# Kernel tuning notes

Hardware: AMD Instinct MI355X
Metric: run time of the kernel (lower is better)

The kernel has to match this reference:

```python
import jax, jax.numpy as jnp
import numpy as np

SLOT = 32
MLP_H = 128
N_SLOTS = 7
N_ITER = 3
EPS = 1e-8
SCALE = SLOT ** -0.5
LN_EPS = 1e-5  # torch LayerNorm default


def _ln(x, g, b):
    m = jnp.mean(x, axis=-1, keepdims=True)
    v = jnp.var(x, axis=-1, keepdims=True)
    return (x - m) * jax.lax.rsqrt(v + LN_EPS) * g + b


def setup_inputs() -> dict:
    key = jax.random.key(0)
    ks = jax.random.split(key, 16)
    def w(k, shape, fan_in):
        return jax.random.normal(k, shape, jnp.float32) * (1.0 / np.sqrt(fan_in))
    return {
        "inputs": jax.random.normal(ks[0], (64, 4096, MLP_H), jnp.float32),
        "slots_init": jax.random.normal(ks[1], (64, N_SLOTS, SLOT), jnp.float32),
        "ln_in_g": jnp.ones((MLP_H,), jnp.float32),
        "ln_in_b": jnp.zeros((MLP_H,), jnp.float32),
        "Wk": w(ks[2], (SLOT, MLP_H), MLP_H),
        "Wv": w(ks[3], (SLOT, MLP_H), MLP_H),
        "Wq": w(ks[4], (SLOT, SLOT), SLOT),
        "ln_s_g": jnp.ones((SLOT,), jnp.float32),
        "ln_s_b": jnp.zeros((SLOT,), jnp.float32),
        "gru_wi": w(ks[5], (3 * SLOT, SLOT), SLOT),
        "gru_wh": w(ks[6], (3 * SLOT, SLOT), SLOT),
        "gru_bi": jnp.zeros((3 * SLOT,), jnp.float32),
        "gru_bh": jnp.zeros((3 * SLOT,), jnp.float32),
        "ln_m_g": jnp.ones((SLOT,), jnp.float32),
        "ln_m_b": jnp.zeros((SLOT,), jnp.float32),
        "mlp_w1": w(ks[7], (MLP_H, SLOT), SLOT),
        "mlp_b1": jnp.zeros((MLP_H,), jnp.float32),
        "mlp_w2": w(ks[8], (SLOT, MLP_H), MLP_H),
        "mlp_b2": jnp.zeros((SLOT,), jnp.float32),
    }


def _gru_cell(x, h, wi, wh, bi, bh):
    # torch.nn.GRUCell math; gate order r, z, n
    gi = x @ wi.T + bi
    gh = h @ wh.T + bh
    gi_r, gi_z, gi_n = jnp.split(gi, 3, axis=-1)
    gh_r, gh_z, gh_n = jnp.split(gh, 3, axis=-1)
    r = jax.nn.sigmoid(gi_r + gh_r)
    z = jax.nn.sigmoid(gi_z + gh_z)
    n = jnp.tanh(gi_n + r * gh_n)
    return (1.0 - z) * n + z * h


def reference(inputs, slots_init, ln_in_g, ln_in_b, Wk, Wv, Wq, ln_s_g, ln_s_b,
              gru_wi, gru_wh, gru_bi, gru_bh, ln_m_g, ln_m_b,
              mlp_w1, mlp_b1, mlp_w2, mlp_b2):
    x = _ln(inputs, ln_in_g, ln_in_b)           # [B, N, 128]
    k = x @ Wk.T                                # [B, N, 32]
    v = x @ Wv.T                                # [B, N, 32]

    slots = slots_init                          # [B, S, 32]
    attn = None
    for m in range(N_ITER + 1):
        slots_prev = slots
        s = _ln(slots, ln_s_g, ln_s_b)
        q = s @ Wq.T                            # [B, S, 32]
        dots = jnp.einsum('bid,bjd->bij', q, k) * SCALE   # [B, S, N]
        attn = jax.nn.softmax(dots, axis=1) + EPS          # softmax over slots
        attn = attn / jnp.sum(attn, axis=-1, keepdims=True)
        updates = jnp.einsum('bjd,bij->bid', v, attn)      # [B, S, 32]
        slots = _gru_cell(updates, slots_prev, gru_wi, gru_wh, gru_bi, gru_bh)
        h = _ln(slots, ln_m_g, ln_m_b)
        h = jax.nn.relu(h @ mlp_w1.T + mlp_b1) @ mlp_w2.T + mlp_b2
        slots = slots + h
        if m == N_ITER - 1:
            slots = jax.lax.stop_gradient(slots)
    return slots, attn, slots
```

## Files before the change

kernel.cpp:

```cpp
#include <hip/hip_runtime.h>
#include <stdint.h>

#define B_   64
#define N_   4096
#define H_   128
#define S_   7
#define D_   32
#define SCALE_ 0.17677669529663687f
#define EPS_   1e-8f
#define LNEPS_ 1e-5f
#define AUS_ 260

typedef __bf16 bf16x8 __attribute__((ext_vector_type(8)));
typedef float  floatx4 __attribute__((ext_vector_type(4)));

__device__ __forceinline__ uint32_t cvt2(float a, float b){
  union { __bf16 h[2]; uint32_t u; } r;
  r.h[0] = (__bf16)a; r.h[1] = (__bf16)b;
  return r.u;
}
__device__ __forceinline__ float bfLO(uint32_t u){ union{uint32_t i; float f;} x; x.i = u << 16;         return x.f; }
__device__ __forceinline__ float bfHI(uint32_t u){ union{uint32_t i; float f;} x; x.i = u & 0xffff0000u; return x.f; }
__device__ __forceinline__ void up8(uint4 u, float* o){
  o[0]=bfLO(u.x); o[1]=bfHI(u.x); o[2]=bfLO(u.y); o[3]=bfHI(u.y);
  o[4]=bfLO(u.z); o[5]=bfHI(u.z); o[6]=bfLO(u.w); o[7]=bfHI(u.w);
}

__global__ __launch_bounds__(256) void init_w(const float* __restrict__ Wk, const float* __restrict__ Wv,
                                              const float* __restrict__ g,  const float* __restrict__ bta,
                                              uint16_t* __restrict__ fragbuf,
                                              float* __restrict__ c1arr, float* __restrict__ c2arr){
  int tid = blockIdx.x * 256 + threadIdx.x;
  if (blockIdx.x < 4){
    int nt = tid >> 8, kc = (tid >> 6) & 3, l = tid & 63;
    int col = (nt & 1) * 16 + (l & 15);
    int dbase = kc * 32 + (l >> 4) * 8;
    const float* wr = (nt < 2 ? Wk : Wv) + col * 128 + dbase;
    const float* gr = g + dbase;
    uint32_t u[4];
    #pragma unroll
    for (int j = 0; j < 4; ++j)
      u[j] = cvt2(wr[2*j] * gr[2*j], wr[2*j+1] * gr[2*j+1]);
    *reinterpret_cast<uint4*>(fragbuf + (size_t)tid * 8) = make_uint4(u[0], u[1], u[2], u[3]);
  } else {
    int t = threadIdx.x;
    if (t < 128){
      int which = t >> 5, col = t & 31;
      const float* Wb  = (which & 2) ? Wv : Wk;
      const float* vec = (which & 1) ? bta : g;
      float a = 0.f;
      for (int d = 0; d < 128; ++d) a += vec[d] * Wb[col * 128 + d];
      float* dst = (which & 1) ? c2arr : c1arr;
      dst[(which >> 1) * 32 + col] = a;
    }
  }
}

__global__ __launch_bounds__(256) void ln_kv(const float* __restrict__ x,
                                             const uint16_t* __restrict__ fragbuf,
                                             const float* __restrict__ c1arr, const float* __restrict__ c2arr,
                                             uint16_t* __restrict__ kb, uint16_t* __restrict__ vb){
  __shared__ union {
    uint16_t atile[64 * 136];
    float    rep[4352];
  } sh;
  __shared__ float2 stats[32 * 65];
  __shared__ float2 rowstat[64];
  int t = threadIdx.x;
  int l = t & 63, w = t >> 6;
  size_t rowbase = (size_t)blockIdx.x * 64;

  bf16x8 bfr[4][4];
  #pragma unroll
  for (int nt = 0; nt < 4; ++nt)
    #pragma unroll
    for (int kc = 0; kc < 4; ++kc)
      bfr[nt][kc] = *reinterpret_cast<const bf16x8*>(fragbuf + (((nt * 4 + kc) * 64 + l) * 8));

  float c1c[4], c2c[4];
  #pragma unroll
  for (int nt = 0; nt < 4; ++nt){
    int colk = (nt & 1) * 16 + (l & 15);
    c1c[nt] = c1arr[(nt >> 1) * 32 + colk];
    c2c[nt] = c2arr[(nt >> 1) * 32 + colk];
  }

  const float4* xp = reinterpret_cast<const float4*>(x + rowbase * H_);
  #pragma unroll
  for (int k = 0; k < 8; ++k){
    float4 v = xp[k * 256 + t];
    int row = 8 * k + (t >> 5);
    uint32_t lo = cvt2(v.x, v.y);
    uint32_t hi = cvt2(v.z, v.w);
    *reinterpret_cast<uint2*>(&sh.atile[row * 136 + (t & 31) * 4]) = make_uint2(lo, hi);
    float s  = v.x + v.y + v.z + v.w;
    float s2 = v.x*v.x + v.y*v.y + v.z*v.z + v.w*v.w;
    stats[(t & 31) * 65 + row] = make_float2(s, s2);
  }
  __syncthreads();

  {
    int row = t >> 2, q = t & 3;
    float s = 0.f, s2 = 0.f;
    #pragma unroll
    for (int j = 0; j < 8; ++j){
      float2 p = stats[(q * 8 + j) * 65 + row];
      s += p.x; s2 += p.y;
    }
    s  += __shfl_xor(s, 1);  s2 += __shfl_xor(s2, 1);
    s  += __shfl_xor(s, 2);  s2 += __shfl_xor(s2, 2);
    if (q == 0){
      float mean = s * (1.f / 128.f);
      float var  = s2 * (1.f / 128.f) - mean * mean;
      float rstd = rsqrtf(var + LNEPS_);
      rowstat[row] = make_float2(rstd, -mean * rstd);
    }
  }
  __syncthreads();

  floatx4 acc[4] = {{0,0,0,0},{0,0,0,0},{0,0,0,0},{0,0,0,0}};
  #pragma unroll
  for (int kc = 0; kc < 4; ++kc){
    bf16x8 afr = *reinterpret_cast<const bf16x8*>(
        &sh.atile[(w * 16 + (l & 15)) * 136 + kc * 32 + (l >> 4) * 8]);
    #pragma unroll
    for (int nt = 0; nt < 4; ++nt)
      acc[nt] = __builtin_amdgcn_mfma_f32_16x16x32_bf16(afr, bfr[nt][kc], acc[nt], 0, 0, 0);
  }
  __syncthreads();

  #pragma unroll
  for (int j = 0; j < 4; ++j){
    int rloc = w * 16 + (l >> 4) * 4 + j;
    float2 ab = rowstat[rloc];
    #pragma unroll
    for (int nt = 0; nt < 4; ++nt){
      int base = (nt < 2) ? 0 : 2176;
      int gc = (nt & 1) * 16 + (l & 15);
      sh.rep[base + rloc * 34 + gc] = fmaf(ab.x, acc[nt][j], fmaf(ab.y, c1c[nt], c2c[nt]));
    }
  }
  __syncthreads();

  uint32_t* kout = reinterpret_cast<uint32_t*>(kb + rowbase * 32);
  uint32_t* vout = reinterpret_cast<uint32_t*>(vb + rowbase * 32);
  #pragma unroll
  for (int it = 0; it < 4; ++it){
    int lin = it * 256 + t;
    int row = lin >> 4, wd = (lin & 15) * 2;
    kout[lin] = cvt2(sh.rep[row * 34 + wd],        sh.rep[row * 34 + wd + 1]);
    vout[lin] = cvt2(sh.rep[2176 + row * 34 + wd], sh.rep[2176 + row * 34 + wd + 1]);
  }
}

__global__ __launch_bounds__(256) void attn_acc(const uint16_t* __restrict__ kb, const uint16_t* __restrict__ vb,
                                                const float* __restrict__ qbuf,
                                                float* __restrict__ updbuf, float* __restrict__ rowsumbuf,
                                                float* __restrict__ aub, int lastIter){
  __shared__ float au[S_ * AUS_];
  __shared__ float vtile[256 * 32];
  int b = blockIdx.y, chunk = blockIdx.x, t = threadIdx.x;

  int rem = t % 56, prt = t / 56;
  int pi = rem >> 3, pc4 = rem & 7;

  float rs[7];
  #pragma unroll
  for (int i = 0; i < 7; ++i) rs[i] = 0.f;
  float ux = 0.f, uy = 0.f, uz = 0.f, uw = 0.f;

  const float* qb = qbuf + b * (S_ * D_);

  for (int tile = 0; tile < 2; ++tile){
    int j = chunk * 512 + tile * 256 + t;
    const uint4* kr = reinterpret_cast<const uint4*>(kb + ((size_t)b * N_ + j) * 32);
    float kf[32];
    #pragma unroll
    for (int p = 0; p < 4; ++p) up8(kr[p], kf + p * 8);

    float dv[7];
    #pragma unroll
    for (int i = 0; i < 7; ++i){
      const float* qr = qb + i * 32;
      float a = 0.f;
      #pragma unroll
      for (int c = 0; c < 32; ++c) a += qr[c] * kf[c];
      dv[i] = a * SCALE_;
    }
    float mx = dv[0];
    #pragma unroll
    for (int i = 1; i < 7; ++i) mx = fmaxf(mx, dv[i]);
    float p[7]; float sum = 0.f;
    #pragma unroll
    for (int i = 0; i < 7; ++i){ p[i] = __expf(dv[i] - mx); sum += p[i]; }
    float inv = 1.f / sum;
    #pragma unroll
    for (int i = 0; i < 7; ++i){
      p[i] = p[i] * inv + EPS_;
      rs[i] += p[i];
      au[i * AUS_ + t] = p[i];
    }
    if (lastIter){
      #pragma unroll
      for (int i = 0; i < 7; ++i) aub[(size_t)(b * S_ + i) * N_ + j] = p[i];
    }
    const uint4* vr = reinterpret_cast<const uint4*>(vb + ((size_t)b * N_ + j) * 32);
    float vf[32];
    #pragma unroll
    for (int p4 = 0; p4 < 4; ++p4) up8(vr[p4], vf + p4 * 8);
    #pragma unroll
    for (int q4 = 0; q4 < 8; ++q4){
      int blk = q4 ^ (t & 7);
      float4 vv = make_float4(vf[q4*4], vf[q4*4+1], vf[q4*4+2], vf[q4*4+3]);
      *reinterpret_cast<float4*>(&vtile[t * 32 + blk * 4]) = vv;
    }
    __syncthreads();

    if (t < 224){
      const float* aur = au + pi * AUS_ + prt * 64;
      #pragma unroll 4
      for (int jj0 = 0; jj0 < 64; jj0 += 4){
        float4 a4 = *reinterpret_cast<const float4*>(&aur[jj0]);
        int jj = prt * 64 + jj0;
        #pragma unroll
        for (int q = 0; q < 4; ++q){
          float a = (q == 0) ? a4.x : (q == 1) ? a4.y : (q == 2) ? a4.z : a4.w;
          int blk = pc4 ^ ((jj + q) & 7);
          float4 vv = *reinterpret_cast<const float4*>(&vtile[(jj + q) * 32 + blk * 4]);
          ux += a * vv.x; uy += a * vv.y; uz += a * vv.z; uw += a * vv.w;
        }
      }
    }
    __syncthreads();
  }

  #pragma unroll
  for (int i = 0; i < 7; ++i) au[i * AUS_ + t] = rs[i];
  __syncthreads();
  for (int off = 128; off >= 1; off >>= 1){
    if (t < off){
      #pragma unroll
      for (int i = 0; i < 7; ++i) au[i * AUS_ + t] += au[i * AUS_ + t + off];
    }
    __syncthreads();
  }
  if (t < 7) atomicAdd(&rowsumbuf[b * S_ + t], au[t * AUS_]);
  if (t < 224){
    float* up = updbuf + (size_t)(b * S_ + pi) * 32 + pc4 * 4;
    atomicAdd(up + 0, ux); atomicAdd(up + 1, uy);
    atomicAdd(up + 2, uz); atomicAdd(up + 3, uw);
  }
}

__global__ __launch_bounds__(256) void slot_update(
    const float* __restrict__ slots_init,
    float* __restrict__ slotsbuf, float* __restrict__ updbuf, float* __restrict__ rowsumbuf,
    float* __restrict__ qbuf,
    const float* __restrict__ Wq,
    const float* __restrict__ lnsg, const float* __restrict__ lnsb,
    const float* __restrict__ gwi, const float* __restrict__ gwh,
    const float* __restrict__ gbi, const float* __restrict__ gbh,
    const float* __restrict__ lnmg, const float* __restrict__ lnmb,
    const float* __restrict__ w1, const float* __restrict__ b1,
    const float* __restrict__ w2, const float* __restrict__ b2,
    int doC, int doA)
{
  int b = blockIdx.x, t = threadIdx.x;
  int i = t >> 5, c = t & 31;
  __shared__ float sPrev[224], sU[224], sNew[224], sT[224], hM[896];
  float snew = 0.f;

  if (doC){
    if (t < 224){
      sPrev[t] = slotsbuf[b * 224 + t];
      sU[t] = updbuf[b * 224 + t] / rowsumbuf[b * S_ + i];
    }
    __syncthreads();
    if (t < 224){
      float gi[3], gh[3];
      #pragma unroll
      for (int x3 = 0; x3 < 3; ++x3){
        int gg = x3 * 32 + c;
        float ai = gbi[gg], ah = gbh[gg];
        #pragma unroll
        for (int d = 0; d < 32; ++d){
          ai += sU[i * 32 + d]    * gwi[gg * 32 + d];
          ah += sPrev[i * 32 + d] * gwh[gg * 32 + d];
        }
        gi[x3] = ai; gh[x3] = ah;
      }
      float r = 1.f / (1.f + __expf(-(gi[0] + gh[0])));
      float z = 1.f / (1.f + __expf(-(gi[1] + gh[1])));
      float n = tanhf(gi[2] + r * gh[2]);
      snew = (1.f - z) * n + z * sPrev[t];
      sNew[t] = snew;
    }
    __syncthreads();
    if (t < 224){
      float mu = 0.f, sq = 0.f;
      #pragma unroll
      for (int d = 0; d < 32; ++d){ float v = sNew[i * 32 + d]; mu += v; sq += v * v; }
      mu *= (1.f / 32.f);
      float var = sq * (1.f / 32.f) - mu * mu;
      float rstd = rsqrtf(var + LNEPS_);
      sT[t] = (snew - mu) * rstd * lnmg[c] + lnmb[c];
    }
    __syncthreads();
    if (t < 224){
      #pragma unroll
      for (int kk = 0; kk < 4; ++kk){
        int hc = c + kk * 32;
        float a = b1[hc];
        #pragma unroll
        for (int d = 0; d < 32; ++d) a += sT[i * 32 + d] * w1[hc * 32 + d];
        hM[i * 128 + hc] = fmaxf(a, 0.f);
      }
    }
    __syncthreads();
    if (t < 224){
      float a0 = 0.f, a1 = 0.f, a2 = 0.f, a3 = 0.f;
      for (int hh = 0; hh < 128; hh += 4){
        a0 += hM[i * 128 + hh    ] * w2[c * 128 + hh    ];
        a1 += hM[i * 128 + hh + 1] * w2[c * 128 + hh + 1];
        a2 += hM[i * 128 + hh + 2] * w2[c * 128 + hh + 2];
        a3 += hM[i * 128 + hh + 3] * w2[c * 128 + hh + 3];
      }
      snew = snew + b2[c] + ((a0 + a1) + (a2 + a3));
      slotsbuf[b * 224 + t] = snew;
      sNew[t] = snew;
    }
  } else {
    if (t < 224){
      snew = slots_init[b * 224 + t];
      slotsbuf[b * 224 + t] = snew;
      sNew[t] = snew;
    }
  }

  if (doA){
    __syncthreads();
    if (t < 224){
      float mu = 0.f, sq = 0.f;
      #pragma unroll
      for (int d = 0; d < 32; ++d){ float v = sNew[i * 32 + d]; mu += v; sq += v * v; }
      mu *= (1.f / 32.f);
      float var = sq * (1.f / 32.f) - mu * mu;
      float rstd = rsqrtf(var + LNEPS_);
      sT[t] = (sNew[t] - mu) * rstd * lnsg[c] + lnsb[c];
    }
    __syncthreads();
    if (t < 224){
      float a = 0.f;
      #pragma unroll
      for (int d = 0; d < 32; ++d) a += sT[i * 32 + d] * Wq[c * 32 + d];
      qbuf[b * 224 + t] = a;
      updbuf[b * 224 + t] = 0.f;
    }
    if (t < 7) rowsumbuf[b * S_ + t] = 0.f;
  }
}

__global__ __launch_bounds__(256) void finalize(
    const float* __restrict__ slotsbuf, const float* __restrict__ updbuf,
    const float* __restrict__ rowsumbuf, const float* __restrict__ aubuf,
    const float* __restrict__ gwi, const float* __restrict__ gwh,
    const float* __restrict__ gbi, const float* __restrict__ gbh,
    const float* __restrict__ lnmg, const float* __restrict__ lnmb,
    const float* __restrict__ w1, const float* __restrict__ b1,
    const float* __restrict__ w2, const float* __restrict__ b2,
    float* __restrict__ out0, float* __restrict__ out1, float* __restrict__ out2)
{
  int t = threadIdx.x;
  if (blockIdx.x >= 64){
    int blk = blockIdx.x - 64;
    #pragma unroll
    for (int k2 = 0; k2 < 4; ++k2){
      int idx4 = blk * 1024 + k2 * 256 + t;
      int bi = idx4 >> 10;
      float inv = 1.f / rowsumbuf[bi];
      float4 a = reinterpret_cast<const float4*>(aubuf)[idx4];
      reinterpret_cast<float4*>(out1)[idx4] = make_float4(a.x*inv, a.y*inv, a.z*inv, a.w*inv);
    }
    return;
  }
  int b = blockIdx.x;
  int i7 = t >> 5, c = t & 31;
  __shared__ float sPrev[224], sU[224], sNew[224], sT[224], hM[896];
  float snew = 0.f;
  if (t < 224){
    sPrev[t] = slotsbuf[b * 224 + t];
    sU[t] = updbuf[b * 224 + t] / rowsumbuf[b * S_ + i7];
  }
  __syncthreads();
  if (t < 224){
    float gi[3], gh[3];
    #pragma unroll
    for (int x3 = 0; x3 < 3; ++x3){
      int gg = x3 * 32 + c;
      float ai = gbi[gg], ah = gbh[gg];
      #pragma unroll
      for (int d = 0; d < 32; ++d){
        ai += sU[i7 * 32 + d]    * gwi[gg * 32 + d];
        ah += sPrev[i7 * 32 + d] * gwh[gg * 32 + d];
      }
      gi[x3] = ai; gh[x3] = ah;
    }
    float r = 1.f / (1.f + __expf(-(gi[0] + gh[0])));
    float z = 1.f / (1.f + __expf(-(gi[1] + gh[1])));
    float n = tanhf(gi[2] + r * gh[2]);
    snew = (1.f - z) * n + z * sPrev[t];
    sNew[t] = snew;
  }
  __syncthreads();
  if (t < 224){
    float mu = 0.f, sq = 0.f;
    #pragma unroll
    for (int d = 0; d < 32; ++d){ float v = sNew[i7 * 32 + d]; mu += v; sq += v * v; }
    mu *= (1.f / 32.f);
    float var = sq * (1.f / 32.f) - mu * mu;
    float rstd = rsqrtf(var + LNEPS_);
    sT[t] = (snew - mu) * rstd * lnmg[c] + lnmb[c];
  }
  __syncthreads();
  if (t < 224){
    #pragma unroll
    for (int kk = 0; kk < 4; ++kk){
      int hc = c + kk * 32;
      float a = b1[hc];
      #pragma unroll
      for (int d = 0; d < 32; ++d) a += sT[i7 * 32 + d] * w1[hc * 32 + d];
      hM[i7 * 128 + hc] = fmaxf(a, 0.f);
    }
  }
  __syncthreads();
  if (t < 224){
    float a0 = 0.f, a1 = 0.f, a2 = 0.f, a3 = 0.f;
    for (int hh = 0; hh < 128; hh += 4){
      a0 += hM[i7 * 128 + hh    ] * w2[c * 128 + hh    ];
      a1 += hM[i7 * 128 + hh + 1] * w2[c * 128 + hh + 1];
      a2 += hM[i7 * 128 + hh + 2] * w2[c * 128 + hh + 2];
      a3 += hM[i7 * 128 + hh + 3] * w2[c * 128 + hh + 3];
    }
    snew = snew + b2[c] + ((a0 + a1) + (a2 + a3));
    out0[b * 224 + t] = snew;
    out2[b * 224 + t] = snew;
  }
}

extern "C" void kernel_launch(void* const* d_in, const int* in_sizes, int n_in,
                              void* d_out, int out_size, void* d_ws, size_t ws_size,
                              hipStream_t stream)
{
  (void)in_sizes; (void)n_in; (void)out_size; (void)ws_size;
  const float* inp   = (const float*)d_in[0];
  const float* sini  = (const float*)d_in[1];
  const float* lng   = (const float*)d_in[2];
  const float* lnb   = (const float*)d_in[3];
  const float* Wk    = (const float*)d_in[4];
  const float* Wv    = (const float*)d_in[5];
  const float* Wq    = (const float*)d_in[6];
  const float* lnsg  = (const float*)d_in[7];
  const float* lnsb  = (const float*)d_in[8];
  const float* gwi   = (const float*)d_in[9];
  const float* gwh   = (const float*)d_in[10];
  const float* gbi   = (const float*)d_in[11];
  const float* gbh   = (const float*)d_in[12];
  const float* lnmg  = (const float*)d_in[13];
  const float* lnmb  = (const float*)d_in[14];
  const float* w1    = (const float*)d_in[15];
  const float* b1    = (const float*)d_in[16];
  const float* w2    = (const float*)d_in[17];
  const float* b2    = (const float*)d_in[18];

  char* w = (char*)d_ws;
  uint16_t* kbuf   = (uint16_t*)w; w += (size_t)B_ * N_ * 32 * 2;
  uint16_t* vbuf   = (uint16_t*)w; w += (size_t)B_ * N_ * 32 * 2;
  float* qbuf      = (float*)w; w += B_ * 224 * 4;
  float* slotsbuf  = (float*)w; w += B_ * 224 * 4;
  float* updbuf    = (float*)w; w += B_ * 224 * 4;
  float* rowsumbuf = (float*)w; w += B_ * S_ * 4;
  float* aubuf     = (float*)w; w += (size_t)B_ * S_ * N_ * 4;
  uint16_t* fragbuf= (uint16_t*)w; w += 8192 * 2;
  float* c1arr     = (float*)w; w += 64 * 4;
  float* c2arr     = (float*)w; w += 64 * 4;

  float* out0 = (float*)d_out;
  float* out1 = out0 + B_ * S_ * D_;
  float* out2 = out1 + B_ * S_ * N_;

  hipLaunchKernelGGL(init_w, dim3(5), dim3(256), 0, stream, Wk, Wv, lng, lnb, fragbuf, c1arr, c2arr);
  hipLaunchKernelGGL(ln_kv, dim3(4096), dim3(256), 0, stream, inp, fragbuf, c1arr, c2arr, kbuf, vbuf);

  hipLaunchKernelGGL(slot_update, dim3(64), dim3(256), 0, stream,
                     sini, slotsbuf, updbuf, rowsumbuf, qbuf, Wq, lnsg, lnsb,
                     gwi, gwh, gbi, gbh, lnmg, lnmb, w1, b1, w2, b2,
                     0, 1);

  for (int m = 0; m < 4; ++m){
    hipLaunchKernelGGL(attn_acc, dim3(8, 64), dim3(256), 0, stream,
                       kbuf, vbuf, qbuf, updbuf, rowsumbuf, aubuf, (m == 3) ? 1 : 0);
    if (m < 3){
      hipLaunchKernelGGL(slot_update, dim3(64), dim3(256), 0, stream,
                         sini, slotsbuf, updbuf, rowsumbuf, qbuf, Wq, lnsg, lnsb,
                         gwi, gwh, gbi, gbh, lnmg, lnmb, w1, b1, w2, b2,
                         1, 1);
    }
  }

  hipLaunchKernelGGL(finalize, dim3(512), dim3(256), 0, stream,
                     slotsbuf, updbuf, rowsumbuf, aubuf,
                     gwi, gwh, gbi, gbh, lnmg, lnmb, w1, b1, w2, b2,
                     out0, out1, out2);
}
```

Baseline: 184.6 us.

## Compute slot-key dots with bf16 MFMA and reduce row sums via wave shuffles

New measurement: 190.4 us. 3.1% more time.

```diff
diff --git a/kernel.cpp b/kernel.cpp
--- a/kernel.cpp
+++ b/kernel.cpp
@@ -18,6 +18,9 @@
   union { __bf16 h[2]; uint32_t u; } r;
   r.h[0] = (__bf16)a; r.h[1] = (__bf16)b;
   return r.u;
+}
+__device__ __forceinline__ uint16_t f2b(float a){
+  union { __bf16 h; uint16_t u; } r; r.h = (__bf16)a; return r.u;
 }
 __device__ __forceinline__ float bfLO(uint32_t u){ union{uint32_t i; float f;} x; x.i = u << 16;         return x.f; }
 __device__ __forceinline__ float bfHI(uint32_t u){ union{uint32_t i; float f;} x; x.i = u & 0xffff0000u; return x.f; }
@@ -160,50 +163,58 @@
   __shared__ float au[S_ * AUS_];
   __shared__ float vtile[256 * 32];
   int b = blockIdx.y, chunk = blockIdx.x, t = threadIdx.x;
+  int w = t >> 6, l = t & 63;
+  int slot = l & 15, g = l >> 4, d0 = g * 8;
+
+  union { uint16_t u[8]; bf16x8 v; } qa;
+  #pragma unroll
+  for (int jx = 0; jx < 8; ++jx) qa.u[jx] = 0;
+  if (slot < 7){
+    const float* qr = qbuf + b * 224 + slot * 32 + d0;
+    #pragma unroll
+    for (int jx = 0; jx < 8; ++jx) qa.u[jx] = f2b(qr[jx] * SCALE_);
+  }
 
   int rem = t % 56, prt = t / 56;
   int pi = rem >> 3, pc4 = rem & 7;
 
-  float rs[7];
-  #pragma unroll
-  for (int i = 0; i < 7; ++i) rs[i] = 0.f;
+  float rs4[4] = {0.f, 0.f, 0.f, 0.f};
   float ux = 0.f, uy = 0.f, uz = 0.f, uw = 0.f;
 
-  const float* qb = qbuf + b * (S_ * D_);
-
-  for (int tile = 0; tile < 2; ++tile){
-    int j = chunk * 512 + tile * 256 + t;
-    const uint4* kr = reinterpret_cast<const uint4*>(kb + ((size_t)b * N_ + j) * 32);
-    float kf[32];
-    #pragma unroll
-    for (int p = 0; p < 4; ++p) up8(kr[p], kf + p * 8);
-
-    float dv[7];
-    #pragma unroll
-    for (int i = 0; i < 7; ++i){
-      const float* qr = qb + i * 32;
-      float a = 0.f;
-      #pragma unroll
-      for (int c = 0; c < 32; ++c) a += qr[c] * kf[c];
-      dv[i] = a * SCALE_;
-    }
-    float mx = dv[0];
-    #pragma unroll
-    for (int i = 1; i < 7; ++i) mx = fmaxf(mx, dv[i]);
-    float p[7]; float sum = 0.f;
-    #pragma unroll
-    for (int i = 0; i < 7; ++i){ p[i] = __expf(dv[i] - mx); sum += p[i]; }
-    float inv = 1.f / sum;
-    #pragma unroll
-    for (int i = 0; i < 7; ++i){
-      p[i] = p[i] * inv + EPS_;
-      rs[i] += p[i];
-      au[i * AUS_ + t] = p[i];
-    }
-    if (lastIter){
-      #pragma unroll
-      for (int i = 0; i < 7; ++i) aub[(size_t)(b * S_ + i) * N_ + j] = p[i];
-    }
+  for (int pass = 0; pass < 2; ++pass){
+    int jbase = chunk * 512 + pass * 256;
+
+    #pragma unroll
+    for (int tt = 0; tt < 4; ++tt){
+      int jt = (w * 4 + tt) * 16;
+      bf16x8 kfrag = *reinterpret_cast<const bf16x8*>(
+          kb + ((size_t)b * N_ + jbase + jt + slot) * 32 + d0);
+      floatx4 dv = __builtin_amdgcn_mfma_f32_16x16x32_bf16(qa.v, kfrag, (floatx4){0,0,0,0}, 0, 0, 0);
+      float mx;
+      if (g == 0)      mx = fmaxf(fmaxf(dv[0], dv[1]), fmaxf(dv[2], dv[3]));
+      else if (g == 1) mx = fmaxf(fmaxf(dv[0], dv[1]), dv[2]);
+      else             mx = -3.0e38f;
+      mx = fmaxf(mx, __shfl_xor(mx, 16));
+      mx = fmaxf(mx, __shfl_xor(mx, 32));
+      float e0 = 0.f, e1 = 0.f, e2 = 0.f, e3 = 0.f, s = 0.f;
+      if (g < 2){
+        e0 = __expf(dv[0] - mx); e1 = __expf(dv[1] - mx); e2 = __expf(dv[2] - mx);
+        if (g == 0){ e3 = __expf(dv[3] - mx); s = (e0 + e1) + (e2 + e3); }
+        else s = (e0 + e1) + e2;
+      }
+      s += __shfl_xor(s, 16); s += __shfl_xor(s, 32);
+      float inv = 1.f / s;
+      int jloc = jt + slot;
+      if (g < 2){
+        float p0 = e0 * inv + EPS_, p1 = e1 * inv + EPS_, p2 = e2 * inv + EPS_;
+        au[(g * 4 + 0) * AUS_ + jloc] = p0; rs4[0] += p0;
+        au[(g * 4 + 1) * AUS_ + jloc] = p1; rs4[1] += p1;
+        au[(g * 4 + 2) * AUS_ + jloc] = p2; rs4[2] += p2;
+        if (g == 0){ float p3 = e3 * inv + EPS_; au[3 * AUS_ + jloc] = p3; rs4[3] += p3; }
+      }
+    }
+
+    int j = jbase + t;
     const uint4* vr = reinterpret_cast<const uint4*>(vb + ((size_t)b * N_ + j) * 32);
     float vf[32];
     #pragma unroll
@@ -215,6 +226,11 @@
       *reinterpret_cast<float4*>(&vtile[t * 32 + blk * 4]) = vv;
     }
     __syncthreads();
+
+    if (lastIter){
+      #pragma unroll
+      for (int i = 0; i < 7; ++i) aub[(size_t)(b * S_ + i) * N_ + j] = au[i * AUS_ + t];
+    }
 
     if (t < 224){
       const float* aur = au + pi * AUS_ + prt * 64;
@@ -235,16 +251,24 @@
   }
 
   #pragma unroll
-  for (int i = 0; i < 7; ++i) au[i * AUS_ + t] = rs[i];
-  __syncthreads();
-  for (int off = 128; off >= 1; off >>= 1){
-    if (t < off){
-      #pragma unroll
-      for (int i = 0; i < 7; ++i) au[i * AUS_ + t] += au[i * AUS_ + t + off];
-    }
-    __syncthreads();
-  }
-  if (t < 7) atomicAdd(&rowsumbuf[b * S_ + t], au[t * AUS_]);
+  for (int r = 0; r < 4; ++r){
+    float v = rs4[r];
+    v += __shfl_xor(v, 1); v += __shfl_xor(v, 2);
+    v += __shfl_xor(v, 4); v += __shfl_xor(v, 8);
+    rs4[r] = v;
+  }
+  if (slot == 0 && g < 2){
+    if (g == 0){
+      atomicAdd(&rowsumbuf[b * S_ + 0], rs4[0]);
+      atomicAdd(&rowsumbuf[b * S_ + 1], rs4[1]);
+      atomicAdd(&rowsumbuf[b * S_ + 2], rs4[2]);
+      atomicAdd(&rowsumbuf[b * S_ + 3], rs4[3]);
+    } else {
+      atomicAdd(&rowsumbuf[b * S_ + 4], rs4[0]);
+      atomicAdd(&rowsumbuf[b * S_ + 5], rs4[1]);
+      atomicAdd(&rowsumbuf[b * S_ + 6], rs4[2]);
+    }
+  }
   if (t < 224){
     float* up = updbuf + (size_t)(b * S_ + pi) * 32 + pc4 * 4;
     atomicAdd(up + 0, ux); atomicAdd(up + 1, uy);
```
